# Kernel tuning notes

Hardware: AMD Instinct MI355X
Metric: run time of the kernel (lower is better)

Reference implementation:

```python
import jax, jax.numpy as jnp
import numpy as np

WINDOW = 512  # sliding-window size (keys per query, including self)


def setup_inputs() -> dict:
    key = jax.random.key(0)
    ks = jax.random.split(key, 5)
    B, T, C = 2, 8192, 1024
    s = 1.0 / np.sqrt(C)
    return {
        "x": jax.random.normal(ks[0], (B, T, C), dtype=jnp.float32),
        "Wq": jax.random.normal(ks[1], (C, C), dtype=jnp.float32) * s,
        "Wk": jax.random.normal(ks[2], (C, C), dtype=jnp.float32) * s,
        "Wv": jax.random.normal(ks[3], (C, C), dtype=jnp.float32) * s,
        "Wo": jax.random.normal(ks[4], (C, C), dtype=jnp.float32) * s,
    }


def _block_local_attn(q, k, v, window):
    # q,k,v: [B,H,T,D]; causal sliding-window attention, honoring sparsity by
    # attending only to the current and previous block of size `window`.
    B, H, T, D = q.shape
    W = window
    nb = T // W
    scale = 1.0 / jnp.sqrt(jnp.asarray(D, q.dtype))
    qb = q.reshape(B, H, nb, W, D)
    kb = k.reshape(B, H, nb, W, D)
    vb = v.reshape(B, H, nb, W, D)
    # previous block (zero-padded for block 0)
    kp = jnp.pad(kb, ((0, 0), (0, 0), (1, 0), (0, 0), (0, 0)))[:, :, :nb]
    vp = jnp.pad(vb, ((0, 0), (0, 0), (1, 0), (0, 0), (0, 0)))[:, :, :nb]
    k2 = jnp.concatenate([kp, kb], axis=3)  # [B,H,nb,2W,D]
    v2 = jnp.concatenate([vp, vb], axis=3)
    i = jnp.arange(W)[:, None]          # query index within block
    j = jnp.arange(2 * W)[None, :]      # key index (0..W-1 prev, W..2W-1 cur)
    # key global offset = j - W relative to query block start; causal window of
    # size W (self + W-1 previous) <=> i < j <= i + W
    base = (j > i) & (j <= i + W)                                  # [W,2W]
    prev_ok = (jnp.arange(nb)[:, None] > 0) | (jnp.arange(2 * W)[None, :] >= W)
    mask = base[None, :, :] & prev_ok[:, None, :]                  # [nb,W,2W]
    scores = jnp.einsum("bhnqd,bhnkd->bhnqk", qb, k2) * scale
    scores = jnp.where(mask[None, None], scores, jnp.asarray(-1e30, scores.dtype))
    p = jax.nn.softmax(scores, axis=-1)
    out = jnp.einsum("bhnqk,bhnkd->bhnqd", p, v2)
    return out.reshape(B, H, T, D)


def reference(x, Wq, Wk, Wv, Wo):
    B, T, C = x.shape
    H = 16
    D = C // H
    # nn.Linear(y = x @ W^T), bias=False
    q = (x @ Wq.T).reshape(B, T, H, D).transpose(0, 2, 1, 3)
    k = (x @ Wk.T).reshape(B, T, H, D).transpose(0, 2, 1, 3)
    v = (x @ Wv.T).reshape(B, T, H, D).transpose(0, 2, 1, 3)
    out = _block_local_attn(q, k, v, WINDOW)
    out = out.transpose(0, 2, 1, 3).reshape(B, T, C)
    return out @ Wo.T
```

## Files before the change

kernel.cpp:

```cpp
#include <hip/hip_runtime.h>
#include <hip/hip_bf16.h>
#include <stdint.h>

typedef __attribute__((ext_vector_type(8))) short short8;
typedef __attribute__((ext_vector_type(4))) float f32x4;
typedef __hip_bfloat16 bf16;

#define AS1 __attribute__((address_space(1)))
#define AS3 __attribute__((address_space(3)))

__device__ __forceinline__ void gl16(const void* g, void* l) {
  __builtin_amdgcn_global_load_lds((const AS1 unsigned int*)g,
                                   (AS3 unsigned int*)l, 16, 0, 0);
}

__device__ __forceinline__ unsigned short bfbits(float x) {
  union { bf16 b; unsigned short u; } c; c.b = __float2bfloat16(x); return c.u;
}

#define SCHED0 __builtin_amdgcn_sched_barrier(0)

__global__ __launch_bounds__(256) void k_cvt(const float* __restrict__ src,
                                             bf16* __restrict__ dst, int n8) {
  int i = blockIdx.x * blockDim.x + threadIdx.x;
  int stride = gridDim.x * blockDim.x;
  for (; i < n8; i += stride) {
    const float4* p = (const float4*)src + (size_t)i * 2;
    float4 a = p[0], b = p[1];
    bf16 tmp[8];
    tmp[0] = __float2bfloat16(a.x); tmp[1] = __float2bfloat16(a.y);
    tmp[2] = __float2bfloat16(a.z); tmp[3] = __float2bfloat16(a.w);
    tmp[4] = __float2bfloat16(b.x); tmp[5] = __float2bfloat16(b.y);
    tmp[6] = __float2bfloat16(b.z); tmp[7] = __float2bfloat16(b.w);
    *(short8*)(dst + (size_t)i * 8) = *(short8*)tmp;
  }
}


#define GEMM_BODY(...)                                                         \
  const int Kd = 1024;                                                         \
  const int nk = 32;                                              \
  __shared__ bf16 As[4][256 * 32];                                             \
  __shared__ bf16 Bs[4][256 * 32];                                             \
  int tid = threadIdx.x;                                                       \
  int lane = tid & 63, wid = tid >> 6;                                         \
  int l15 = lane & 15, hi = lane >> 4;                                         \
  int wm = wid >> 2, wn = wid & 3;                                             \
  f32x4 acc[8][4];                                                             \
  _Pragma("unroll") for (int i = 0; i < 8; i++)                                \
      _Pragma("unroll") for (int j = 0; j < 4; j++)                            \
          acc[i][j] = (f32x4){0.f, 0.f, 0.f, 0.f};                             \
  auto stageA = [&](int slot, int kk) {                                        \
    const bf16* ab = Abase + kk * 32;                                          \
    _Pragma("unroll") for (int pass = 0; pass < 2; pass++) {                   \
      int p = pass * 512 + tid;                                                \
      int row = p >> 2;                                                        \
      int u = (p & 3) ^ ((row >> 1) & 3);                                      \
      gl16(ab + (size_t)row * Kd + u * 8, (char*)(&As[slot][0]) + p * 16);     \
    }                                                                          \
  };                                                                           \
  auto stageB = [&](int slot, int kk) {                                        \
    const bf16* bb = Bbase + kk * 32;                                          \
    _Pragma("unroll") for (int pass = 0; pass < 2; pass++) {                   \
      int p = pass * 512 + tid;                                                \
      int row = p >> 2;                                                        \
      int u = (p & 3) ^ ((row >> 1) & 3);                                      \
      gl16(bb + (size_t)row * Kd + u * 8, (char*)(&Bs[slot][0]) + p * 16);     \
    }                                                                          \
  };                                                                           \
  stageA(0, 0); stageB(0, 0);                                                  \
  stageA(1, 1); stageB(1, 1);                                                  \
  stageA(2, 2); stageB(2, 2);                                                  \
  asm volatile("s_waitcnt vmcnt(8)" ::: "memory");                             \
  SCHED0; __builtin_amdgcn_s_barrier(); SCHED0;                                \
  int sw = ((l15 >> 1) & 3) << 4;                                              \
  int arow = wm * 128 + l15;                                                   \
  int brow = wn * 64 + l15;                                                    \
  short8 ax[4], ahi[4], bcur[4], axn[4], bn[4];                                \
  _Pragma("unroll") for (int mf = 0; mf < 4; mf++)                             \
      ax[mf] = *(const short8*)((const char*)(&As[0][0]) +                     \
                                (((arow + mf * 16) * 64 + hi * 16) ^ sw));     \
  _Pragma("unroll") for (int nf = 0; nf < 4; nf++)                             \
      bcur[nf] = *(const short8*)((const char*)(&Bs[0][0]) +                   \
                                  (((brow + nf * 16) * 64 + hi * 16) ^ sw));   \
  _Pragma("unroll 2") for (int t = 0; t < nk; ++t) {                           \
    int s = t & 3, sn = (t + 1) & 3;                                           \
    const char* Ab = (const char*)(&As[s][0]);                                 \
          \
    _Pragma("unroll") for (int mf = 0; mf < 4; mf++)                           \
        ahi[mf] = *(const short8*)(Ab +                                        \
            (((arow + 64 + mf * 16) * 64 + hi * 16) ^ sw));                    \
    if (t + 3 < nk) stageA((t + 3) & 3, t + 3);                                \
    SCHED0;                                                                    \
    __builtin_amdgcn_s_setprio(1);                                             \
    _Pragma("unroll") for (int mf = 0; mf < 4; mf++)                           \
        _Pragma("unroll") for (int nf = 0; nf < 4; nf++)                       \
            acc[mf][nf] = __builtin_amdgcn_mfma_f32_16x16x32_bf16(             \
                ax[mf], bcur[nf], acc[mf][nf], 0, 0, 0);                       \
    __builtin_amdgcn_s_setprio(0);                                             \
    SCHED0;                                                                    \
         \
    if (t + 1 < nk) {                                                          \
      if (t + 3 < nk)      asm volatile("s_waitcnt vmcnt(6)" ::: "memory");    \
      else if (t + 2 < nk) asm volatile("s_waitcnt vmcnt(4)" ::: "memory");    \
      else                 asm volatile("s_waitcnt vmcnt(0)" ::: "memory");    \
      SCHED0; __builtin_amdgcn_s_barrier(); SCHED0;                            \
      if (t + 3 < nk) stageB((t + 3) & 3, t + 3);                              \
      const char* AbN = (const char*)(&As[sn][0]);                             \
      const char* BbN = (const char*)(&Bs[sn][0]);                             \
      _Pragma("unroll") for (int mf = 0; mf < 4; mf++)                         \
          axn[mf] = *(const short8*)(AbN +                                     \
              (((arow + mf * 16) * 64 + hi * 16) ^ sw));                       \
      _Pragma("unroll") for (int nf = 0; nf < 4; nf++)                         \
          bn[nf] = *(const short8*)(BbN +                                      \
              (((brow + nf * 16) * 64 + hi * 16) ^ sw));                       \
      SCHED0;                                                                  \
    }                                                                          \
    __builtin_amdgcn_s_setprio(1);                                             \
    _Pragma("unroll") for (int mf = 0; mf < 4; mf++)                           \
        _Pragma("unroll") for (int nf = 0; nf < 4; nf++)                       \
            acc[mf + 4][nf] = __builtin_amdgcn_mfma_f32_16x16x32_bf16(         \
                ahi[mf], bcur[nf], acc[mf + 4][nf], 0, 0, 0);                  \
    __builtin_amdgcn_s_setprio(0);                                             \
    SCHED0;                                                                    \
    if (t + 1 < nk) {                                                          \
      __builtin_amdgcn_s_barrier(); SCHED0;                                    \
      _Pragma("unroll") for (int i = 0; i < 4; i++) {                          \
        ax[i] = axn[i]; bcur[i] = bn[i];                                       \
      }                                                                        \
    }                                                                          \
  }                                                                            \
  __VA_ARGS__

__global__ __launch_bounds__(512, 2) void k_qkv_gemm(
    const bf16* __restrict__ X, const bf16* __restrict__ Wq,
    const bf16* __restrict__ Wk, const bf16* __restrict__ Wv,
    bf16* __restrict__ Q, bf16* __restrict__ K, bf16* __restrict__ V) {
  int bid = blockIdx.x;
  int wsel = bid >> 8;
  int rem = bid & 255;
  int mt = rem & 63;
  int nt = rem >> 6;
  const bf16* W = (wsel == 0) ? Wq : (wsel == 1) ? Wk : Wv;
  bf16* Dst = (wsel == 0) ? Q : (wsel == 1) ? K : V;
  const bf16* Abase = X + (size_t)mt * 256 * 1024;
  const bf16* Bbase = W + (size_t)nt * 256 * 1024;
  GEMM_BODY({
    _Pragma("unroll") for (int mf = 0; mf < 8; mf++) {
      _Pragma("unroll") for (int r = 0; r < 4; r++) {
        int row = mt * 256 + wm * 128 + mf * 16 + hi * 4 + r;
        int b = row >> 13;
        int tok = row & 8191;
        _Pragma("unroll") for (int nf = 0; nf < 4; nf++) {
          int col = nt * 256 + wn * 64 + nf * 16 + l15;
          int h = col >> 6;
          int d = col & 63;
          Dst[((size_t)(b * 16 + h) * 8192 + tok) * 64 + d] =
              __float2bfloat16(acc[mf][nf][r]);
        }
      }
    }
  })
}

__global__ __launch_bounds__(512, 2) void k_out_gemm(
    const bf16* __restrict__ A, const bf16* __restrict__ Wo,
    float* __restrict__ Out) {
  int bid = blockIdx.x;
  int mt = bid & 63;
  int nt = bid >> 6;
  const bf16* Abase = A + (size_t)mt * 256 * 1024;
  const bf16* Bbase = Wo + (size_t)nt * 256 * 1024;
  GEMM_BODY({
    _Pragma("unroll") for (int mf = 0; mf < 8; mf++) {
      _Pragma("unroll") for (int r = 0; r < 4; r++) {
        int row = mt * 256 + wm * 128 + mf * 16 + hi * 4 + r;
        _Pragma("unroll") for (int nf = 0; nf < 4; nf++) {
          int col = nt * 256 + wn * 64 + nf * 16 + l15;
          Out[(size_t)row * 1024 + col] = acc[mf][nf][r];
        }
      }
    }
  })
}

__global__ __launch_bounds__(256) void k_vtrans(const bf16* __restrict__ V,
                                                bf16* __restrict__ VT) {
  const int T = 8192;
  __shared__ bf16 tile[64][72];
  int bid = blockIdx.x;
  int tb = bid & 127;
  int bh = bid >> 7;
  int t0 = tb * 64;
  int tid = threadIdx.x;
  int r = tid >> 2, c4 = tid & 3;
  const bf16* src = V + ((size_t)bh * T + t0 + r) * 64 + c4 * 16;
  short8 a = *(const short8*)src;
  short8 b2 = *(const short8*)(src + 8);
#pragma unroll
  for (int e = 0; e < 8; e++) tile[r][c4 * 16 + e] = ((bf16*)&a)[e];
#pragma unroll
  for (int e = 0; e < 8; e++) tile[r][c4 * 16 + 8 + e] = ((bf16*)&b2)[e];
  __syncthreads();
  alignas(16) bf16 o[16];
#pragma unroll
  for (int e = 0; e < 16; e++) o[e] = tile[c4 * 16 + e][r];
  bf16* dst = VT + ((size_t)bh * 64 + r) * T + t0 + c4 * 16;
  *(short8*)dst = *(short8*)o;
  *(short8*)(dst + 8) = *((short8*)o + 1);
}

__global__ __launch_bounds__(512) void k_attn(
    const bf16* __restrict__ Q, const bf16* __restrict__ K,
    const bf16* __restrict__ VT, bf16* __restrict__ ATT) {
  const int T = 8192;
  __shared__ bf16 Ks[2][64 * 64];
  __shared__ bf16 Vs[2][64 * 64];
  __shared__ bf16 Ps[8][16 * 64];
  int bid = blockIdx.x;
  int qt = bid & 63;
  int bh = bid >> 6;
  int b = bh >> 4, h = bh & 15;
  int tid = threadIdx.x;
  int lane = tid & 63, wid = tid >> 6;
  int l15 = lane & 15, hi = lane >> 4;
  int q0 = qt * 128;
  int qw = q0 + wid * 16;

  short8 bq[2];
  const bf16* qp = Q + ((size_t)bh * T + qw + l15) * 64 + hi * 8;
  bq[0] = *(const short8*)qp;
  bq[1] = *(const short8*)(qp + 32);

  const bf16* Kbh = K + (size_t)bh * T * 64;
  const bf16* Vbh = VT + (size_t)bh * 64 * T;

  auto stage = [&](int bb, int c0) {
    int p = tid;
    int row = p >> 3;
    int u = (p & 7) ^ (row & 7);
    gl16(Kbh + ((size_t)(c0 + row)) * 64 + u * 8, (char*)(&Ks[bb][0]) + p * 16);
    gl16(Vbh + (size_t)row * T + c0 + u * 8, (char*)(&Vs[bb][0]) + p * 16);
  };

  int cstart = q0 - 512; if (cstart < 0) cstart = 0;
  int nch = (q0 + 128 - cstart) >> 6;

  f32x4 oacc[4];
#pragma unroll
  for (int c = 0; c < 4; c++) oacc[c] = (f32x4){0.f, 0.f, 0.f, 0.f};
  float ssum = 0.f;

  stage(0, cstart);
  __syncthreads();
  int buf = 0;
  for (int ci = 0; ci < nch; ci++) {
    int c0 = cstart + (ci << 6);
    if (ci + 1 < nch) stage(buf ^ 1, c0 + 64);
    f32x4 sacc[4];
#pragma unroll
    for (int ks = 0; ks < 4; ks++) sacc[ks] = (f32x4){0.f, 0.f, 0.f, 0.f};
#pragma unroll
    for (int dh = 0; dh < 2; dh++) {
#pragma unroll
      for (int ks = 0; ks < 4; ks++) {
        int krow = ks * 16 + l15;
        int boff = ((krow * 64 + dh * 32 + hi * 8) * 2) ^ ((krow & 7) << 4);
        short8 ak = *(const short8*)((const char*)(&Ks[buf][0]) + boff);
        sacc[ks] = __builtin_amdgcn_mfma_f32_16x16x32_bf16(ak, bq[dh], sacc[ks], 0, 0, 0);
      }
    }
    float pv[4][4];
    float psum = 0.f;
    bool fullok = (c0 + 63 <= qw) && (c0 + 512 >= qw + 16);
    if (fullok) {
#pragma unroll
      for (int ks = 0; ks < 4; ks++)
#pragma unroll
        for (int r = 0; r < 4; r++) {
          float p = __expf(fmaf(sacc[ks][r], 0.125f, -12.0f));
          pv[ks][r] = p;
          psum += p;
        }
    } else {
      int qg = qw + l15;
#pragma unroll
      for (int ks = 0; ks < 4; ks++)
#pragma unroll
        for (int r = 0; r < 4; r++) {
          int jg = c0 + ks * 16 + hi * 4 + r;
          float p = __expf(fmaf(sacc[ks][r], 0.125f, -12.0f));
          p = ((jg <= qg) && (jg > qg - 512)) ? p : 0.f;
          pv[ks][r] = p;
          psum += p;
        }
    }
    psum += __shfl_xor(psum, 16);
    psum += __shfl_xor(psum, 32);
    ssum += psum;
#pragma unroll
    for (int ks = 0; ks < 4; ks++) {
      unsigned int lo = (unsigned)bfbits(pv[ks][0]) | ((unsigned)bfbits(pv[ks][1]) << 16);
      unsigned int hi2 = (unsigned)bfbits(pv[ks][2]) | ((unsigned)bfbits(pv[ks][3]) << 16);
      int j0 = ks * 16 + hi * 4;
      int a0 = ((l15 * 64 + j0) * 2) ^ ((l15 & 7) << 4);
      int a1 = ((l15 * 64 + j0 + 2) * 2) ^ ((l15 & 7) << 4);
      *(unsigned int*)((char*)(&Ps[wid][0]) + a0) = lo;
      *(unsigned int*)((char*)(&Ps[wid][0]) + a1) = hi2;
    }
    short8 ap[2];
#pragma unroll
    for (int js = 0; js < 2; js++) {
      int a = ((l15 * 64 + js * 32 + hi * 8) * 2) ^ ((l15 & 7) << 4);
      ap[js] = *(const short8*)((const char*)(&Ps[wid][0]) + a);
    }
#pragma unroll
    for (int js = 0; js < 2; js++)
#pragma unroll
      for (int c = 0; c < 4; c++) {
        int vrow = c * 16 + l15;
        int boff = ((vrow * 64 + js * 32 + hi * 8) * 2) ^ ((vrow & 7) << 4);
        short8 bv = *(const short8*)((const char*)(&Vs[buf][0]) + boff);
        oacc[c] = __builtin_amdgcn_mfma_f32_16x16x32_bf16(ap[js], bv, oacc[c], 0, 0, 0);
      }
    __syncthreads();
    buf ^= 1;
  }
  float inv = 1.f / ssum;
#pragma unroll
  for (int r = 0; r < 4; r++) {
    float f = __shfl(inv, hi * 4 + r);
    int tok = qw + hi * 4 + r;
    bf16* dst = ATT + ((size_t)b * 8192 + tok) * 1024 + h * 64;
#pragma unroll
    for (int c = 0; c < 4; c++)
      dst[c * 16 + l15] = __float2bfloat16(oacc[c][r] * f);
  }
}

extern "C" void kernel_launch(void* const* d_in, const int* in_sizes, int n_in,
                              void* d_out, int out_size, void* d_ws, size_t ws_size,
                              hipStream_t stream) {
  const float* x  = (const float*)d_in[0];
  const float* wq = (const float*)d_in[1];
  const float* wk = (const float*)d_in[2];
  const float* wv = (const float*)d_in[3];
  const float* wo = (const float*)d_in[4];
  float* out = (float*)d_out;

  char* ws = (char*)d_ws;
  const size_t SZ_X = (size_t)16384 * 1024 * 2;
  const size_t SZ_W = (size_t)1024 * 1024 * 2;
  size_t off = 0;
  bf16* xb  = (bf16*)(ws + off); off += SZ_X;
  bf16* wqb = (bf16*)(ws + off); off += SZ_W;
  bf16* wkb = (bf16*)(ws + off); off += SZ_W;
  bf16* wvb = (bf16*)(ws + off); off += SZ_W;
  bf16* wob = (bf16*)(ws + off); off += SZ_W;
  bf16* qb  = (bf16*)(ws + off); off += SZ_X;
  bf16* kb  = (bf16*)(ws + off); off += SZ_X;
  bf16* vb  = (bf16*)(ws + off); off += SZ_X;
  bf16* vtb = (bf16*)(ws + off); off += SZ_X;
  bf16* att = xb;

  k_cvt<<<2048, 256, 0, stream>>>(x, xb, 16384 * 1024 / 8);
  k_cvt<<<512, 256, 0, stream>>>(wq, wqb, 1024 * 1024 / 8);
  k_cvt<<<512, 256, 0, stream>>>(wk, wkb, 1024 * 1024 / 8);
  k_cvt<<<512, 256, 0, stream>>>(wv, wvb, 1024 * 1024 / 8);
  k_cvt<<<512, 256, 0, stream>>>(wo, wob, 1024 * 1024 / 8);
  k_qkv_gemm<<<768, 512, 0, stream>>>(xb, wqb, wkb, wvb, qb, kb, vb);
  k_vtrans<<<4096, 256, 0, stream>>>(vb, vtb);
  k_attn<<<2048, 512, 0, stream>>>(qb, kb, vtb, att);
  k_out_gemm<<<256, 512, 0, stream>>>(att, wob, out);
}
```

Measured before the change: 291.3 us.

## Deepen attention K/V staging to four buffers and merge weight conversions

```diff
diff --git a/kernel.cpp b/kernel.cpp
--- a/kernel.cpp
+++ b/kernel.cpp
@@ -34,6 +34,26 @@
     tmp[6] = __float2bfloat16(b.z); tmp[7] = __float2bfloat16(b.w);
     *(short8*)(dst + (size_t)i * 8) = *(short8*)tmp;
   }
+}
+
+__global__ __launch_bounds__(256) void k_cvtw(
+    const float* __restrict__ w0, const float* __restrict__ w1,
+    const float* __restrict__ w2, const float* __restrict__ w3,
+    bf16* __restrict__ d0, bf16* __restrict__ d1,
+    bf16* __restrict__ d2, bf16* __restrict__ d3) {
+  int gi = blockIdx.x * 256 + threadIdx.x;
+  int m = gi >> 17;
+  int i = gi & 131071;
+  const float* src = (m == 0) ? w0 : (m == 1) ? w1 : (m == 2) ? w2 : w3;
+  bf16* dst = (m == 0) ? d0 : (m == 1) ? d1 : (m == 2) ? d2 : d3;
+  const float4* p = (const float4*)src + (size_t)i * 2;
+  float4 a = p[0], b = p[1];
+  bf16 tmp[8];
+  tmp[0] = __float2bfloat16(a.x); tmp[1] = __float2bfloat16(a.y);
+  tmp[2] = __float2bfloat16(a.z); tmp[3] = __float2bfloat16(a.w);
+  tmp[4] = __float2bfloat16(b.x); tmp[5] = __float2bfloat16(b.y);
+  tmp[6] = __float2bfloat16(b.z); tmp[7] = __float2bfloat16(b.w);
+  *(short8*)(dst + (size_t)i * 8) = *(short8*)tmp;
 }
 
 
@@ -214,8 +234,8 @@
     const bf16* __restrict__ Q, const bf16* __restrict__ K,
     const bf16* __restrict__ VT, bf16* __restrict__ ATT) {
   const int T = 8192;
-  __shared__ bf16 Ks[2][64 * 64];
-  __shared__ bf16 Vs[2][64 * 64];
+  __shared__ bf16 Ks[4][64 * 64];
+  __shared__ bf16 Vs[4][64 * 64];
   __shared__ bf16 Ps[8][16 * 64];
   int bid = blockIdx.x;
   int qt = bid & 63;
@@ -252,11 +272,16 @@
   float ssum = 0.f;
 
   stage(0, cstart);
-  __syncthreads();
-  int buf = 0;
+  stage(1, cstart + 64);
   for (int ci = 0; ci < nch; ci++) {
     int c0 = cstart + (ci << 6);
-    if (ci + 1 < nch) stage(buf ^ 1, c0 + 64);
+    int buf = ci & 3;
+    if (ci + 2 < nch) stage((ci + 2) & 3, c0 + 128);
+    SCHED0;
+    if (ci + 2 < nch)      asm volatile("s_waitcnt vmcnt(4)" ::: "memory");
+    else if (ci + 1 < nch) asm volatile("s_waitcnt vmcnt(2)" ::: "memory");
+    else                   asm volatile("s_waitcnt vmcnt(0)" ::: "memory");
+    SCHED0; __builtin_amdgcn_s_barrier(); SCHED0;
     f32x4 sacc[4];
 #pragma unroll
     for (int ks = 0; ks < 4; ks++) sacc[ks] = (f32x4){0.f, 0.f, 0.f, 0.f};
@@ -323,8 +348,6 @@
         short8 bv = *(const short8*)((const char*)(&Vs[buf][0]) + boff);
         oacc[c] = __builtin_amdgcn_mfma_f32_16x16x32_bf16(ap[js], bv, oacc[c], 0, 0, 0);
       }
-    __syncthreads();
-    buf ^= 1;
   }
   float inv = 1.f / ssum;
 #pragma unroll
@@ -364,10 +387,7 @@
   bf16* att = xb;
 
   k_cvt<<<2048, 256, 0, stream>>>(x, xb, 16384 * 1024 / 8);
-  k_cvt<<<512, 256, 0, stream>>>(wq, wqb, 1024 * 1024 / 8);
-  k_cvt<<<512, 256, 0, stream>>>(wk, wkb, 1024 * 1024 / 8);
-  k_cvt<<<512, 256, 0, stream>>>(wv, wvb, 1024 * 1024 / 8);
-  k_cvt<<<512, 256, 0, stream>>>(wo, wob, 1024 * 1024 / 8);
+  k_cvtw<<<2048, 256, 0, stream>>>(wq, wk, wv, wo, wqb, wkb, wvb, wob);
   k_qkv_gemm<<<768, 512, 0, stream>>>(xb, wqb, wkb, wvb, qb, kb, vb);
   k_vtrans<<<4096, 256, 0, stream>>>(vb, vtb);
   k_attn<<<2048, 512, 0, stream>>>(qb, kb, vtb, att);
```

New measurement: 295.8 us. No clear change (+1.5%).
